# Optimization experiments

Hardware: AMD Instinct MI355X
Metric: run time of the kernel (lower is better)

## Reference

```python
import jax, jax.numpy as jnp
import numpy as np

B, S, E = 2, 2048, 1024
N_HEADS = 16
HEAD_DIM = E // N_HEADS  # 64
ATTN_SCALE = 1.0 / np.sqrt(E)  # NOTE: original scales by 1/sqrt(hidden_dim_phi), not head_dim
ROPE_BASE = 10000.0


def _rope(t):
    # t: (B, H, S, D) with D = HEAD_DIM; interleaved-pair RoPE (torchtune-style)
    d = t.shape[-1]
    s = t.shape[-2]
    inv_freq = 1.0 / (ROPE_BASE ** (jnp.arange(0, d, 2, dtype=jnp.float32) / d))  # (D/2,)
    ang = jnp.arange(s, dtype=jnp.float32)[:, None] * inv_freq[None, :]  # (S, D/2)
    cos, sin = jnp.cos(ang), jnp.sin(ang)  # (S, D/2)
    tp = t.reshape(t.shape[:-1] + (d // 2, 2))
    te, to = tp[..., 0], tp[..., 1]  # (B,H,S,D/2)
    oe = te * cos - to * sin
    oo = te * sin + to * cos
    return jnp.stack([oe, oo], axis=-1).reshape(t.shape)


def setup_inputs() -> dict:
    key = jax.random.key(0)
    ks = jax.random.split(key, 5)
    std = 0.02
    return {
        "x": jax.random.normal(ks[0], (B, S, E), dtype=jnp.float32),
        "W_q": jax.random.normal(ks[1], (E, E), dtype=jnp.float32) * std,
        "W_k": jax.random.normal(ks[2], (E, E), dtype=jnp.float32) * std,
        "W_v": jax.random.normal(ks[3], (E, E), dtype=jnp.float32) * std,
        "W_o": jax.random.normal(ks[4], (E, E), dtype=jnp.float32) * std,
    }


def reference(x, W_q, W_k, W_v, W_o):
    b, s, e = x.shape
    hd = e // N_HEADS
    # projections -> (B, H, S, D)
    def proj(w):
        return (x @ w).reshape(b, s, N_HEADS, hd).transpose(0, 2, 1, 3)
    q = _rope(proj(W_q))
    k = _rope(proj(W_k))
    v = proj(W_v)
    scores = jnp.einsum('bhsd,bhtd->bhst', q, k) * ATTN_SCALE  # (B,H,S,S)
    causal = jnp.triu(jnp.ones((s, s), dtype=bool), k=1)
    scores = jnp.where(causal, -jnp.inf, scores)
    probs = jax.nn.softmax(scores, axis=-1)  # dropout is identity in eval mode
    out = jnp.einsum('bhst,bhtd->bhsd', probs, v)
    out = out.transpose(0, 2, 1, 3).reshape(b, s, e)
    return out @ W_o
```

## Files before the change

kernel.cpp:

```cpp
#include <hip/hip_runtime.h>
#include <hip/hip_bf16.h>

#define S_LEN 2048
#define E_DIM 1024
#define NH 16
#define HD 64
#define ATTN_SCALE 0.03125f
#define QSCALE_L2E 0.045084312f

typedef __attribute__((ext_vector_type(8))) short short8;
typedef __attribute__((ext_vector_type(8))) unsigned short ushort8;
typedef __attribute__((ext_vector_type(4))) unsigned short ushort4_t;
typedef __attribute__((ext_vector_type(4))) float f32x4;
typedef __attribute__((ext_vector_type(16))) float f32x16;
typedef __attribute__((ext_vector_type(4))) float f4;
typedef __attribute__((ext_vector_type(4))) unsigned int uint4v;

__device__ __forceinline__ float bf2f(unsigned short u) {
    unsigned int x = ((unsigned int)u) << 16;
    return __builtin_bit_cast(float, x);
}
__device__ __forceinline__ unsigned short f2bf(float f) {
    unsigned int x = __builtin_bit_cast(unsigned int, f);
    x += 0x7FFFu + ((x >> 16) & 1u);
    return (unsigned short)(x >> 16);
}
__device__ __forceinline__ float exp2_fast(float x) {
    float r;
    asm("v_exp_f32 %0, %1" : "=v"(r) : "v"(x));
    return r;
}
__device__ __forceinline__ void gload16(const unsigned short* g, unsigned short* l) {
    __builtin_amdgcn_global_load_lds(
        (__attribute__((address_space(1))) void*)g,
        (__attribute__((address_space(3))) void*)l, 16, 0, 0);
}

__global__ __launch_bounds__(256) void k_convert(const float* __restrict__ x,
                                                 unsigned short* __restrict__ xb) {
    size_t i = ((size_t)blockIdx.x * 256 + threadIdx.x) * 8;
    f4 a = *(const f4*)(x + i);
    f4 b = *(const f4*)(x + i + 4);
    ushort8 o;
    o[0] = f2bf(a[0]); o[1] = f2bf(a[1]); o[2] = f2bf(a[2]); o[3] = f2bf(a[3]);
    o[4] = f2bf(b[0]); o[5] = f2bf(b[1]); o[6] = f2bf(b[2]); o[7] = f2bf(b[3]);
    *(ushort8*)(xb + i) = o;
}

__global__ __launch_bounds__(256) void k_transw(const float* W0, const float* W1,
                                                const float* W2, const float* W3,
                                                unsigned short* T0, unsigned short* T1,
                                                unsigned short* T2, unsigned short* T3) {
    const float* W; unsigned short* T;
    switch (blockIdx.z) {
        case 0: W = W0; T = T0; break;
        case 1: W = W1; T = T1; break;
        case 2: W = W2; T = T2; break;
        default: W = W3; T = T3; break;
    }
    __shared__ float tile[32][33];
    int tx = threadIdx.x, ty = threadIdx.y;
    int bx = blockIdx.x * 32, by = blockIdx.y * 32;
#pragma unroll
    for (int i = 0; i < 4; i++)
        tile[ty + i * 8][tx] = W[(size_t)(by + ty + i * 8) * E_DIM + bx + tx];
    __syncthreads();
#pragma unroll
    for (int i = 0; i < 4; i++)
        T[(size_t)(bx + ty + i * 8) * E_DIM + by + tx] = f2bf(tile[tx][ty + i * 8]);
}

__global__ __launch_bounds__(256) void k_rope_table(float* __restrict__ cosT,
                                                    float* __restrict__ sinT) {
    int idx = blockIdx.x * 256 + threadIdx.x;
    int s = idx >> 5, j = idx & 31;
    float inv = expf(-(float)j * (9.210340371976184f / 32.f));
    float ang = (float)s * inv;
    cosT[idx] = cosf(ang);
    sinT[idx] = sinf(ang);
}

template <int BM, int BN, int NBN, bool QKV3>
__global__ __launch_bounds__(256, 3)
void k_gemmN(const unsigned short* __restrict__ A,
             const unsigned short* __restrict__ B,
             unsigned short* __restrict__ Qo,
             unsigned short* __restrict__ Ko,
             unsigned short* __restrict__ Vto,
             float* __restrict__ Fo,
             const float* __restrict__ cosT,
             const float* __restrict__ sinT) {
    constexpr int THREADS = 256;
    constexpr int WM = BM / 2, WN = BN / 2;
    constexpr int FM = WM / 16, FN = WN / 16;
    constexpr int NT = E_DIM / 64;
    constexpr int AR = BM * 8 / THREADS;
    constexpr int BR = BN * 8 / THREADS;
    constexpr int STG = AR + BR;
    constexpr int NWG = (4096 / BM) * NBN;
    __shared__ unsigned short Al[2][BM * 64];
    __shared__ unsigned short Bl[2][BN * 64];
    int tid = threadIdx.x, lane = tid & 63, wid = tid >> 6;
    int l15 = lane & 15, lg = lane >> 4;
    int wr = wid >> 1, wc = wid & 1;
    int orig = blockIdx.y * NBN + blockIdx.x;
    int wg = (orig & 7) * (NWG / 8) + (orig >> 3);
    int bm = wg / NBN, bn = wg % NBN;

    auto stage = [&](int buf, int k0) {
#pragma unroll
        for (int i = 0; i < AR; i++) {
            int r = i * (THREADS / 8) + wid * 8 + (lane >> 3);
            int cs = (lane & 7) ^ (r & 7);
            gload16(A + (size_t)(bm * BM + r) * E_DIM + k0 + cs * 8,
                    &Al[buf][i * (THREADS * 8) + wid * 512]);
        }
#pragma unroll
        for (int i = 0; i < BR; i++) {
            int r = i * (THREADS / 8) + wid * 8 + (lane >> 3);
            int cs = (lane & 7) ^ (r & 7);
            gload16(B + (size_t)(bn * BN + r) * E_DIM + k0 + cs * 8,
                    &Bl[buf][i * (THREADS * 8) + wid * 512]);
        }
    };

    f32x4 acc[FM][FN] = {};
    stage(0, 0);
    for (int t = 0; t < NT; t++) {
        int cur = t & 1;
        if (t + 1 < NT) {
            stage(cur ^ 1, (t + 1) * 64);
            asm volatile("s_waitcnt vmcnt(%0)" :: "n"(STG) : "memory");
        } else {
            asm volatile("s_waitcnt vmcnt(0)" ::: "memory");
        }
        __builtin_amdgcn_s_barrier();
        __builtin_amdgcn_sched_barrier(0);
#pragma unroll
        for (int ks = 0; ks < 2; ks++) {
            short8 af[FM], bfv[FN];
#pragma unroll
            for (int m = 0; m < FM; m++) {
                int r = wr * WM + m * 16 + l15;
                int gc = ks * 4 + lg;
                af[m] = *(const short8*)&Al[cur][r * 64 + ((gc ^ (r & 7)) << 3)];
            }
#pragma unroll
            for (int n = 0; n < FN; n++) {
                int r = wc * WN + n * 16 + l15;
                int gc = ks * 4 + lg;
                bfv[n] = *(const short8*)&Bl[cur][r * 64 + ((gc ^ (r & 7)) << 3)];
            }
            __builtin_amdgcn_s_setprio(1);
#pragma unroll
            for (int m = 0; m < FM; m++)
#pragma unroll
                for (int n = 0; n < FN; n++)
                    acc[m][n] = __builtin_amdgcn_mfma_f32_16x16x32_bf16(
                        af[m], bfv[n], acc[m][n], 0, 0, 0);
            __builtin_amdgcn_s_setprio(0);
        }
        __builtin_amdgcn_s_barrier();
    }
#pragma unroll
    for (int m = 0; m < FM; m++) {
        int r0 = bm * BM + wr * WM + m * 16 + lg * 4;
#pragma unroll
        for (int n = 0; n < FN; n++) {
            int colg = bn * BN + wc * WN + n * 16 + l15;
            if (QKV3) {
                int z = colg >> 10, c1 = colg & 1023;
                if (z == 2) {
                    int h = c1 >> 6, d = c1 & 63;
                    int bb = r0 >> 11, s = r0 & 2047;
                    ushort4_t p;
#pragma unroll
                    for (int r = 0; r < 4; r++) p[r] = f2bf(acc[m][n][r]);
                    *(ushort4_t*)(Vto + (((size_t)((bb * 16 + h) * 64 + d)) << 11) + s) = p;
                } else {
                    unsigned short* T = z ? Ko : Qo;
                    int dl = c1 & 63, j = dl >> 1;
                    float sgn = (dl & 1) ? 1.f : -1.f;
                    float scq = z ? 1.f : QSCALE_L2E;
#pragma unroll
                    for (int r = 0; r < 4; r++) {
                        int row = r0 + r, s = row & 2047;
                        float c = cosT[s * 32 + j], sn = sinT[s * 32 + j];
                        float v = acc[m][n][r];
                        float p = __shfl_xor(v, 1);
                        T[(size_t)row * E_DIM + c1] = f2bf((v * c + sgn * p * sn) * scq);
                    }
                }
            } else {
#pragma unroll
                for (int r = 0; r < 4; r++)
                    Fo[(size_t)(r0 + r) * E_DIM + colg] = acc[m][n][r];
            }
        }
    }
}

__global__ __launch_bounds__(128, 2)
void k_attn32(const unsigned short* __restrict__ Q,
              const unsigned short* __restrict__ K,
              const unsigned short* __restrict__ Vt,
              unsigned short* __restrict__ O) {
    __shared__ unsigned short K_lds[2][4096];
    __shared__ unsigned short V_lds[2][4096];
    int tid = threadIdx.x, lane = tid & 63, wid = tid >> 6;
    int l31 = lane & 31, hi = lane >> 5;
    int orig = blockIdx.y * 32 + blockIdx.x;
    int xcd = orig & 7, idx = orig >> 3;
    int u = idx & 31, v = idx >> 5;
    int bh = xcd * 4 + v;
    int p = (v & 1) ? (31 - u) : u;
    int b = bh >> 4, h = bh & 15;
    const size_t base_qk = (size_t)b * S_LEN * E_DIM + (size_t)h * HD;
    const unsigned short* Vbh = Vt + ((size_t)(bh * 64) << 11);

    auto stageK = [&](int buf, int kt) {
#pragma unroll
        for (int i = 0; i < 4; i++) {
            int r = i * 16 + (tid >> 3);
            int cs = (tid & 7) ^ (r & 7);
            gload16(K + base_qk + (size_t)(kt * 64 + r) * E_DIM + cs * 8,
                    &K_lds[buf][i * 1024 + tid * 8]);
        }
    };
    auto stageV = [&](int buf, int kt) {
#pragma unroll
        for (int i = 0; i < 4; i++) {
            int r = i * 16 + (tid >> 3);
            int cs = (tid & 7) ^ (r & 7);
            gload16(Vbh + (size_t)r * 2048 + kt * 64 + cs * 8,
                    &V_lds[buf][i * 1024 + tid * 8]);
        }
    };

    int q_glob = p * 64 + wid * 32 + l31;
    const unsigned short* Qb = Q + base_qk + (size_t)q_glob * E_DIM;
    short8 qf[4];
#pragma unroll
    for (int s = 0; s < 4; s++)
        qf[s] = *(const short8*)(Qb + s * 16 + hi * 8);

    f32x16 ot0 = {}, ot1 = {};
    float m_i = -1e30f, l_i = 0.f;
    int nkt = p + 1;
    int swz = l31 & 7;
    stageK(0, 0);
    stageV(0, 0);
    asm volatile("s_waitcnt vmcnt(0)" ::: "memory");
    __builtin_amdgcn_s_barrier();
    __builtin_amdgcn_sched_barrier(0);
    int cur = 0;
    for (int kt = 0; kt < nkt; ++kt) {
        if (kt + 1 < nkt) {
            stageK(cur ^ 1, kt + 1);
            stageV(cur ^ 1, kt + 1);
        }
        f32x16 st0 = {}, st1 = {};
        __builtin_amdgcn_s_setprio(1);
#pragma unroll
        for (int s = 0; s < 4; s++) {
            int c = ((s * 2 + hi) ^ swz) << 3;
            short8 ka0 = *(const short8*)&K_lds[cur][l31 * 64 + c];
            short8 ka1 = *(const short8*)&K_lds[cur][(32 + l31) * 64 + c];
            st0 = __builtin_amdgcn_mfma_f32_32x32x16_bf16(ka0, qf[s], st0, 0, 0, 0);
            st1 = __builtin_amdgcn_mfma_f32_32x32x16_bf16(ka1, qf[s], st1, 0, 0, 0);
        }
        __builtin_amdgcn_s_setprio(0);
        float p0[16], p1[16];
        float vmax = -1e30f;
        if (kt == nkt - 1) {
#pragma unroll
            for (int r = 0; r < 16; r++) {
                int kg = kt * 64 + (r & 3) + 8 * (r >> 2) + 4 * hi;
                float v0 = (kg > q_glob) ? -1e30f : st0[r];
                float v1 = (kg + 32 > q_glob) ? -1e30f : st1[r];
                p0[r] = v0; p1[r] = v1;
                vmax = fmaxf(vmax, fmaxf(v0, v1));
            }
        } else {
#pragma unroll
            for (int r = 0; r < 16; r++) {
                p0[r] = st0[r]; p1[r] = st1[r];
                vmax = fmaxf(vmax, fmaxf(st0[r], st1[r]));
            }
        }
        vmax = fmaxf(vmax, __shfl_xor(vmax, 32));
        float m_new = fmaxf(m_i, vmax);
        float corr = exp2_fast(m_i - m_new);
        float rs = 0.f;
#pragma unroll
        for (int r = 0; r < 16; r++) {
            p0[r] = exp2_fast(p0[r] - m_new);
            p1[r] = exp2_fast(p1[r] - m_new);
            rs += p0[r] + p1[r];
        }
        rs += __shfl_xor(rs, 32);
        l_i = l_i * corr + rs;
        m_i = m_new;
#pragma unroll
        for (int r = 0; r < 16; r++) { ot0[r] *= corr; ot1[r] *= corr; }
        unsigned int pk0[8], pk1[8];
#pragma unroll
        for (int i = 0; i < 8; i++) {
            asm("v_cvt_pk_bf16_f32 %0, %1, %2"
                : "=v"(pk0[i]) : "v"(p0[2 * i]), "v"(p0[2 * i + 1]));
            asm("v_cvt_pk_bf16_f32 %0, %1, %2"
                : "=v"(pk1[i]) : "v"(p1[2 * i]), "v"(p1[2 * i + 1]));
        }
        bool ishi = hi != 0;
        __builtin_amdgcn_s_setprio(1);
#pragma unroll
        for (int kk = 0; kk < 4; kk++) {
            const unsigned int* pkt = (kk & 2) ? pk1 : pk0;
            int off = (kk & 1) * 4;
            unsigned int a  = pkt[off + 0], b2 = pkt[off + 1];
            unsigned int c2 = pkt[off + 2], d2 = pkt[off + 3];
            unsigned int sa = __shfl_xor(a, 32),  sb = __shfl_xor(b2, 32);
            unsigned int sc = __shfl_xor(c2, 32), sd = __shfl_xor(d2, 32);
            uint4v w;
            w[0] = ishi ? sc : a;  w[1] = ishi ? sd : b2;
            w[2] = ishi ? c2 : sa; w[3] = ishi ? d2 : sb;
            short8 pf = __builtin_bit_cast(short8, w);
            int cv = ((kk * 2 + hi) ^ swz) << 3;
            short8 va0 = *(const short8*)&V_lds[cur][l31 * 64 + cv];
            short8 va1 = *(const short8*)&V_lds[cur][(32 + l31) * 64 + cv];
            ot0 = __builtin_amdgcn_mfma_f32_32x32x16_bf16(va0, pf, ot0, 0, 0, 0);
            ot1 = __builtin_amdgcn_mfma_f32_32x32x16_bf16(va1, pf, ot1, 0, 0, 0);
        }
        __builtin_amdgcn_s_setprio(0);
        asm volatile("s_waitcnt vmcnt(0)" ::: "memory");
        __builtin_amdgcn_s_barrier();
        __builtin_amdgcn_sched_barrier(0);
        cur ^= 1;
    }
    __builtin_amdgcn_s_barrier();
    float linv = 1.f / l_i;
    unsigned short* scb = &K_lds[0][0] + wid * 2304;
#pragma unroll
    for (int i = 0; i < 8; i++) {
        int d = 2 * (i & 1) + 8 * (i >> 1) + 4 * hi;
        unsigned int w0, w1;
        float a0 = ot0[2 * i] * linv, a1 = ot0[2 * i + 1] * linv;
        float b0 = ot1[2 * i] * linv, b1 = ot1[2 * i + 1] * linv;
        asm("v_cvt_pk_bf16_f32 %0, %1, %2" : "=v"(w0) : "v"(a0), "v"(a1));
        asm("v_cvt_pk_bf16_f32 %0, %1, %2" : "=v"(w1) : "v"(b0), "v"(b1));
        *(unsigned int*)&scb[l31 * 72 + d] = w0;
        *(unsigned int*)&scb[l31 * 72 + 32 + d] = w1;
    }
    asm volatile("s_waitcnt lgkmcnt(0)" ::: "memory");
    __builtin_amdgcn_sched_barrier(0);
    int qr = lane >> 1, half = (lane & 1) * 32;
    unsigned short* Ob = O + base_qk + (size_t)(p * 64 + wid * 32 + qr) * E_DIM;
#pragma unroll
    for (int j = 0; j < 4; j++) {
        short8 vv = *(const short8*)&scb[qr * 72 + half + j * 8];
        *(short8*)(Ob + half + j * 8) = vv;
    }
}

extern "C" void kernel_launch(void* const* d_in, const int* in_sizes, int n_in,
                              void* d_out, int out_size, void* d_ws, size_t ws_size,
                              hipStream_t stream) {
    (void)in_sizes; (void)n_in; (void)out_size; (void)ws_size;
    const float* x  = (const float*)d_in[0];
    const float* Wq = (const float*)d_in[1];
    const float* Wk = (const float*)d_in[2];
    const float* Wv = (const float*)d_in[3];
    const float* Wo = (const float*)d_in[4];

    unsigned short* us = (unsigned short*)d_ws;
    unsigned short* xb    = us;
    unsigned short* WqkvT = us + 4194304;
    unsigned short* WoT   = us + 7340032;
    unsigned short* Qb    = us + 8388608;
    unsigned short* Kb    = us + 12582912;
    unsigned short* Vt    = us + 16777216;
    unsigned short* AO    = us + 20971520;
    float* cosT = (float*)((char*)d_ws + 50331648);
    float* sinT = cosT + 65536;

    k_convert<<<2048, 256, 0, stream>>>(x, xb);
    k_transw<<<dim3(32, 32, 4), dim3(32, 8), 0, stream>>>(
        Wq, Wk, Wv, Wo, WqkvT, WqkvT + 1048576, WqkvT + 2097152, WoT);
    k_rope_table<<<256, 256, 0, stream>>>(cosT, sinT);
    k_gemmN<128, 64, 48, true><<<dim3(48, 32), 256, 0, stream>>>(
        xb, WqkvT, Qb, Kb, Vt, nullptr, cosT, sinT);
    k_attn32<<<dim3(32, 32), 128, 0, stream>>>(Qb, Kb, Vt, AO);
    k_gemmN<128, 64, 16, false><<<dim3(16, 32), 256, 0, stream>>>(
        AO, WoT, nullptr, nullptr, nullptr, (float*)d_out, cosT, sinT);
}
```

Measured before the change: 117.7 us.

## Merge prep kernels, retile QKV GEMM, and restructure attention to 128-query blocks

Folds the x conversion, weight transpose and RoPE table kernels into a single prep launch to cut launch overhead. Replaces the double-buffered 128x64 QKV GEMM with a simpler single-buffered 128x128 tile using K-steps of 32 and barriers each step. Rewrites attention so each 4-wave block handles 128 queries sharing one K/V stage, with single-buffered K and V split-staged across phases. Waves whose rows are fully masked skip work. This trades double-buffer prefetch for more K/V reuse per block and fewer blocks, and risks exposed load latency and more barriers.

```diff
diff --git a/kernel.cpp b/kernel.cpp
--- a/kernel.cpp
+++ b/kernel.cpp
@@ -36,60 +36,142 @@
         (__attribute__((address_space(3))) void*)l, 16, 0, 0);
 }
 
-__global__ __launch_bounds__(256) void k_convert(const float* __restrict__ x,
-                                                 unsigned short* __restrict__ xb) {
-    size_t i = ((size_t)blockIdx.x * 256 + threadIdx.x) * 8;
-    f4 a = *(const f4*)(x + i);
-    f4 b = *(const f4*)(x + i + 4);
-    ushort8 o;
-    o[0] = f2bf(a[0]); o[1] = f2bf(a[1]); o[2] = f2bf(a[2]); o[3] = f2bf(a[3]);
-    o[4] = f2bf(b[0]); o[5] = f2bf(b[1]); o[6] = f2bf(b[2]); o[7] = f2bf(b[3]);
-    *(ushort8*)(xb + i) = o;
-}
-
-__global__ __launch_bounds__(256) void k_transw(const float* W0, const float* W1,
-                                                const float* W2, const float* W3,
-                                                unsigned short* T0, unsigned short* T1,
-                                                unsigned short* T2, unsigned short* T3) {
-    const float* W; unsigned short* T;
-    switch (blockIdx.z) {
-        case 0: W = W0; T = T0; break;
-        case 1: W = W1; T = T1; break;
-        case 2: W = W2; T = T2; break;
-        default: W = W3; T = T3; break;
-    }
-    __shared__ float tile[32][33];
-    int tx = threadIdx.x, ty = threadIdx.y;
-    int bx = blockIdx.x * 32, by = blockIdx.y * 32;
-#pragma unroll
-    for (int i = 0; i < 4; i++)
-        tile[ty + i * 8][tx] = W[(size_t)(by + ty + i * 8) * E_DIM + bx + tx];
-    __syncthreads();
-#pragma unroll
-    for (int i = 0; i < 4; i++)
-        T[(size_t)(bx + ty + i * 8) * E_DIM + by + tx] = f2bf(tile[tx][ty + i * 8]);
-}
-
-__global__ __launch_bounds__(256) void k_rope_table(float* __restrict__ cosT,
-                                                    float* __restrict__ sinT) {
-    int idx = blockIdx.x * 256 + threadIdx.x;
-    int s = idx >> 5, j = idx & 31;
-    float inv = expf(-(float)j * (9.210340371976184f / 32.f));
-    float ang = (float)s * inv;
-    cosT[idx] = cosf(ang);
-    sinT[idx] = sinf(ang);
-}
-
-template <int BM, int BN, int NBN, bool QKV3>
+__global__ __launch_bounds__(256) void k_prep(const float* __restrict__ x,
+                                              unsigned short* __restrict__ xb,
+                                              const float* W0, const float* W1,
+                                              const float* W2, const float* W3,
+                                              unsigned short* Tqkv,
+                                              unsigned short* Twout,
+                                              float* __restrict__ cosT,
+                                              float* __restrict__ sinT) {
+    int bid = blockIdx.x;
+    int tid = threadIdx.x;
+    if (bid < 2048) {
+        size_t i = ((size_t)bid * 256 + tid) * 8;
+        f4 a = *(const f4*)(x + i);
+        f4 b = *(const f4*)(x + i + 4);
+        ushort8 o;
+        o[0] = f2bf(a[0]); o[1] = f2bf(a[1]); o[2] = f2bf(a[2]); o[3] = f2bf(a[3]);
+        o[4] = f2bf(b[0]); o[5] = f2bf(b[1]); o[6] = f2bf(b[2]); o[7] = f2bf(b[3]);
+        *(ushort8*)(xb + i) = o;
+    } else if (bid < 2304) {
+        int idx = (bid - 2048) * 256 + tid;
+        int s = idx >> 5, j = idx & 31;
+        float inv = expf(-(float)j * (9.210340371976184f / 32.f));
+        float ang = (float)s * inv;
+        cosT[idx] = cosf(ang);
+        sinT[idx] = sinf(ang);
+    } else {
+        int t = bid - 2304;
+        int bx = (t & 31) * 32, by = ((t >> 5) & 31) * 32, z = t >> 10;
+        const float* W; unsigned short* T;
+        switch (z) {
+            case 0: W = W0; T = Tqkv; break;
+            case 1: W = W1; T = Tqkv + 1048576; break;
+            case 2: W = W2; T = Tqkv + 2097152; break;
+            default: W = W3; T = Twout; break;
+        }
+        __shared__ float tile[32][33];
+        int tx = tid & 31, ty = tid >> 5;
+#pragma unroll
+        for (int i = 0; i < 4; i++)
+            tile[ty + i * 8][tx] = W[(size_t)(by + ty + i * 8) * E_DIM + bx + tx];
+        __syncthreads();
+#pragma unroll
+        for (int i = 0; i < 4; i++)
+            T[(size_t)(bx + ty + i * 8) * E_DIM + by + tx] = f2bf(tile[tx][ty + i * 8]);
+    }
+}
+
 __global__ __launch_bounds__(256, 3)
-void k_gemmN(const unsigned short* __restrict__ A,
+void k_gemm97(const unsigned short* __restrict__ A,
+              const unsigned short* __restrict__ B,
+              unsigned short* __restrict__ Qo,
+              unsigned short* __restrict__ Ko,
+              unsigned short* __restrict__ Vto,
+              const float* __restrict__ cosT,
+              const float* __restrict__ sinT) {
+    constexpr int NBN = 24;
+    constexpr int NWG = 32 * NBN;
+    __shared__ unsigned short Alds[4096];
+    __shared__ unsigned short Blds[4096];
+    int tid = threadIdx.x, lane = tid & 63, wid = tid >> 6;
+    int l15 = lane & 15, lg = lane >> 4;
+    int wr = wid >> 1, wc = wid & 1;
+    int orig = blockIdx.y * NBN + blockIdx.x;
+    int wg = (orig & 7) * (NWG / 8) + (orig >> 3);
+    int bm = wg / NBN, bn = wg % NBN;
+    int c0 = wid * 2, c1c = wid * 2 + 1;
+    int srow0 = c0 * 16 + (lane >> 2);
+    int srow1 = c1c * 16 + (lane >> 2);
+    int scol = (lane & 3) * 8;
+    const unsigned short* As0 = A + (size_t)(bm * 128 + srow0) * E_DIM + scol;
+    const unsigned short* As1 = A + (size_t)(bm * 128 + srow1) * E_DIM + scol;
+    const unsigned short* Bs0 = B + (size_t)(bn * 128 + srow0) * E_DIM + scol;
+    const unsigned short* Bs1 = B + (size_t)(bn * 128 + srow1) * E_DIM + scol;
+    unsigned short* Ad0 = Alds + c0 * 512;
+    unsigned short* Ad1 = Alds + c1c * 512;
+    unsigned short* Bd0 = Blds + c0 * 512;
+    unsigned short* Bd1 = Blds + c1c * 512;
+    f32x4 acc[4][4] = {};
+    for (int k0 = 0; k0 < E_DIM; k0 += 32) {
+        gload16(As0 + k0, Ad0);
+        gload16(As1 + k0, Ad1);
+        gload16(Bs0 + k0, Bd0);
+        gload16(Bs1 + k0, Bd1);
+        __syncthreads();
+        short8 af[4], bfr[4];
+#pragma unroll
+        for (int mf = 0; mf < 4; mf++)
+            af[mf] = *(const short8*)(Alds + (wr * 64 + mf * 16 + l15) * 32 + lg * 8);
+#pragma unroll
+        for (int nf = 0; nf < 4; nf++)
+            bfr[nf] = *(const short8*)(Blds + (wc * 64 + nf * 16 + l15) * 32 + lg * 8);
+#pragma unroll
+        for (int mf = 0; mf < 4; mf++)
+#pragma unroll
+            for (int nf = 0; nf < 4; nf++)
+                acc[mf][nf] = __builtin_amdgcn_mfma_f32_16x16x32_bf16(
+                    af[mf], bfr[nf], acc[mf][nf], 0, 0, 0);
+        __syncthreads();
+    }
+#pragma unroll
+    for (int mf = 0; mf < 4; mf++) {
+        int r0 = bm * 128 + wr * 64 + mf * 16 + lg * 4;
+#pragma unroll
+        for (int nf = 0; nf < 4; nf++) {
+            int colg = bn * 128 + wc * 64 + nf * 16 + l15;
+            int z = colg >> 10, c1 = colg & 1023;
+            if (z == 2) {
+                int h = c1 >> 6, d = c1 & 63;
+                int bb = r0 >> 11, s = r0 & 2047;
+                ushort4_t p;
+#pragma unroll
+                for (int r = 0; r < 4; r++) p[r] = f2bf(acc[mf][nf][r]);
+                *(ushort4_t*)(Vto + (((size_t)((bb * 16 + h) * 64 + d)) << 11) + s) = p;
+            } else {
+                unsigned short* T = z ? Ko : Qo;
+                int dl = c1 & 63, j = dl >> 1;
+                float sgn = (dl & 1) ? 1.f : -1.f;
+                float scq = z ? 1.f : QSCALE_L2E;
+#pragma unroll
+                for (int r = 0; r < 4; r++) {
+                    int row = r0 + r, s = row & 2047;
+                    float c = cosT[s * 32 + j], sn = sinT[s * 32 + j];
+                    float v = acc[mf][nf][r];
+                    float p = __shfl_xor(v, 1);
+                    T[(size_t)row * E_DIM + c1] = f2bf((v * c + sgn * p * sn) * scq);
+                }
+            }
+        }
+    }
+}
+
+template <int BM, int BN, int NBN>
+__global__ __launch_bounds__(256, 3)
+void k_gemmo(const unsigned short* __restrict__ A,
              const unsigned short* __restrict__ B,
-             unsigned short* __restrict__ Qo,
-             unsigned short* __restrict__ Ko,
-             unsigned short* __restrict__ Vto,
-             float* __restrict__ Fo,
-             const float* __restrict__ cosT,
-             const float* __restrict__ sinT) {
+             float* __restrict__ Fo) {
     constexpr int THREADS = 256;
     constexpr int WM = BM / 2, WN = BN / 2;
     constexpr int FM = WM / 16, FN = WN / 16;
@@ -168,178 +250,171 @@
 #pragma unroll
         for (int n = 0; n < FN; n++) {
             int colg = bn * BN + wc * WN + n * 16 + l15;
-            if (QKV3) {
-                int z = colg >> 10, c1 = colg & 1023;
-                if (z == 2) {
-                    int h = c1 >> 6, d = c1 & 63;
-                    int bb = r0 >> 11, s = r0 & 2047;
-                    ushort4_t p;
-#pragma unroll
-                    for (int r = 0; r < 4; r++) p[r] = f2bf(acc[m][n][r]);
-                    *(ushort4_t*)(Vto + (((size_t)((bb * 16 + h) * 64 + d)) << 11) + s) = p;
-                } else {
-                    unsigned short* T = z ? Ko : Qo;
-                    int dl = c1 & 63, j = dl >> 1;
-                    float sgn = (dl & 1) ? 1.f : -1.f;
-                    float scq = z ? 1.f : QSCALE_L2E;
-#pragma unroll
-                    for (int r = 0; r < 4; r++) {
-                        int row = r0 + r, s = row & 2047;
-                        float c = cosT[s * 32 + j], sn = sinT[s * 32 + j];
-                        float v = acc[m][n][r];
-                        float p = __shfl_xor(v, 1);
-                        T[(size_t)row * E_DIM + c1] = f2bf((v * c + sgn * p * sn) * scq);
-                    }
-                }
-            } else {
-#pragma unroll
-                for (int r = 0; r < 4; r++)
-                    Fo[(size_t)(r0 + r) * E_DIM + colg] = acc[m][n][r];
-            }
-        }
-    }
-}
-
-__global__ __launch_bounds__(128, 2)
-void k_attn32(const unsigned short* __restrict__ Q,
-              const unsigned short* __restrict__ K,
-              const unsigned short* __restrict__ Vt,
-              unsigned short* __restrict__ O) {
-    __shared__ unsigned short K_lds[2][4096];
-    __shared__ unsigned short V_lds[2][4096];
+#pragma unroll
+            for (int r = 0; r < 4; r++)
+                Fo[(size_t)(r0 + r) * E_DIM + colg] = acc[m][n][r];
+        }
+    }
+}
+
+__global__ __launch_bounds__(256, 3)
+void k_attn9(const unsigned short* __restrict__ Q,
+             const unsigned short* __restrict__ K,
+             const unsigned short* __restrict__ Vt,
+             unsigned short* __restrict__ O) {
+    __shared__ unsigned short lds[9216];
+    unsigned short* Klds = lds;
+    unsigned short* Vlds = lds + 4096;
     int tid = threadIdx.x, lane = tid & 63, wid = tid >> 6;
     int l31 = lane & 31, hi = lane >> 5;
-    int orig = blockIdx.y * 32 + blockIdx.x;
+    int orig = blockIdx.y * 16 + blockIdx.x;
     int xcd = orig & 7, idx = orig >> 3;
-    int u = idx & 31, v = idx >> 5;
-    int bh = xcd * 4 + v;
-    int p = (v & 1) ? (31 - u) : u;
+    int bh = xcd * 4 + (idx & 3);
+    int j = idx >> 2;
+    int pt = (j < 8) ? (15 - j) : (j - 8);
     int b = bh >> 4, h = bh & 15;
     const size_t base_qk = (size_t)b * S_LEN * E_DIM + (size_t)h * HD;
     const unsigned short* Vbh = Vt + ((size_t)(bh * 64) << 11);
 
-    auto stageK = [&](int buf, int kt) {
-#pragma unroll
-        for (int i = 0; i < 4; i++) {
-            int r = i * 16 + (tid >> 3);
+    int qbase = pt * 128 + wid * 32;
+    int q_glob = qbase + l31;
+    int nkt = 2 * pt + 2;
+
+    const unsigned short* Qb = Q + base_qk + (size_t)q_glob * E_DIM;
+    short8 qf[4];
+#pragma unroll
+    for (int s = 0; s < 4; s++)
+        qf[s] = *(const short8*)(Qb + s * 16 + hi * 8);
+
+    auto stageK = [&](int kt) {
+        const unsigned short* Kb = K + base_qk + (size_t)(kt * 64) * E_DIM;
+#pragma unroll
+        for (int i = 0; i < 2; i++) {
+            int r = i * 32 + (tid >> 3);
             int cs = (tid & 7) ^ (r & 7);
-            gload16(K + base_qk + (size_t)(kt * 64 + r) * E_DIM + cs * 8,
-                    &K_lds[buf][i * 1024 + tid * 8]);
+            gload16(Kb + (size_t)r * E_DIM + cs * 8, Klds + i * 2048 + tid * 8);
         }
     };
-    auto stageV = [&](int buf, int kt) {
-#pragma unroll
-        for (int i = 0; i < 4; i++) {
-            int r = i * 16 + (tid >> 3);
+    auto stageV = [&](int kt) {
+#pragma unroll
+        for (int i = 0; i < 2; i++) {
+            int r = i * 32 + (tid >> 3);
             int cs = (tid & 7) ^ (r & 7);
             gload16(Vbh + (size_t)r * 2048 + kt * 64 + cs * 8,
-                    &V_lds[buf][i * 1024 + tid * 8]);
+                    Vlds + i * 2048 + tid * 8);
         }
     };
-
-    int q_glob = p * 64 + wid * 32 + l31;
-    const unsigned short* Qb = Q + base_qk + (size_t)q_glob * E_DIM;
-    short8 qf[4];
-#pragma unroll
-    for (int s = 0; s < 4; s++)
-        qf[s] = *(const short8*)(Qb + s * 16 + hi * 8);
 
     f32x16 ot0 = {}, ot1 = {};
     float m_i = -1e30f, l_i = 0.f;
-    int nkt = p + 1;
     int swz = l31 & 7;
-    stageK(0, 0);
-    stageV(0, 0);
-    asm volatile("s_waitcnt vmcnt(0)" ::: "memory");
+
+    stageK(0);
+    stageV(0);
+    asm volatile("s_waitcnt vmcnt(2)" ::: "memory");
     __builtin_amdgcn_s_barrier();
     __builtin_amdgcn_sched_barrier(0);
-    int cur = 0;
     for (int kt = 0; kt < nkt; ++kt) {
+        bool active = (kt * 64) <= (qbase + 31);
+        f32x16 st0 = {}, st1 = {};
+        if (active) {
+            __builtin_amdgcn_s_setprio(1);
+#pragma unroll
+            for (int s = 0; s < 4; s++) {
+                int c = ((s * 2 + hi) ^ swz) << 3;
+                short8 ka0 = *(const short8*)&Klds[l31 * 64 + c];
+                short8 ka1 = *(const short8*)&Klds[(32 + l31) * 64 + c];
+                st0 = __builtin_amdgcn_mfma_f32_32x32x16_bf16(ka0, qf[s], st0, 0, 0, 0);
+                st1 = __builtin_amdgcn_mfma_f32_32x32x16_bf16(ka1, qf[s], st1, 0, 0, 0);
+            }
+            __builtin_amdgcn_s_setprio(0);
+        }
+        __builtin_amdgcn_s_barrier();
+        if (kt + 1 < nkt) stageK(kt + 1);
+        unsigned int pk0[8], pk1[8];
+        if (active) {
+            float p0[16], p1[16];
+            float vmax = -1e30f;
+            bool domask = (kt * 64 + 63) > qbase;
+            if (domask) {
+#pragma unroll
+                for (int r = 0; r < 16; r++) {
+                    int kg = kt * 64 + (r & 3) + 8 * (r >> 2) + 4 * hi;
+                    float v0 = (kg > q_glob) ? -1e30f : st0[r];
+                    float v1 = (kg + 32 > q_glob) ? -1e30f : st1[r];
+                    p0[r] = v0; p1[r] = v1;
+                    vmax = fmaxf(vmax, fmaxf(v0, v1));
+                }
+            } else {
+#pragma unroll
+                for (int r = 0; r < 16; r++) {
+                    p0[r] = st0[r]; p1[r] = st1[r];
+                    vmax = fmaxf(vmax, fmaxf(st0[r], st1[r]));
+                }
+            }
+            vmax = fmaxf(vmax, __shfl_xor(vmax, 32));
+            float m_new = fmaxf(m_i, vmax);
+            float corr = exp2_fast(m_i - m_new);
+            float rs = 0.f;
+#pragma unroll
+            for (int r = 0; r < 16; r++) {
+                p0[r] = exp2_fast(p0[r] - m_new);
+                p1[r] = exp2_fast(p1[r] - m_new);
+                rs += p0[r] + p1[r];
+            }
+            rs += __shfl_xor(rs, 32);
+            l_i = l_i * corr + rs;
+            m_i = m_new;
+#pragma unroll
+            for (int r = 0; r < 16; r++) { ot0[r] *= corr; ot1[r] *= corr; }
+#pragma unroll
+            for (int i = 0; i < 8; i++) {
+                asm("v_cvt_pk_bf16_f32 %0, %1, %2"
+                    : "=v"(pk0[i]) : "v"(p0[2 * i]), "v"(p0[2 * i + 1]));
+                asm("v_cvt_pk_bf16_f32 %0, %1, %2"
+                    : "=v"(pk1[i]) : "v"(p1[2 * i]), "v"(p1[2 * i + 1]));
+            }
+        }
+        if (kt + 1 < nkt)
+            asm volatile("s_waitcnt vmcnt(2)" ::: "memory");
+        else
+            asm volatile("s_waitcnt vmcnt(0)" ::: "memory");
+        __builtin_amdgcn_s_barrier();
+        __builtin_amdgcn_sched_barrier(0);
+        if (active) {
+            bool ishi = hi != 0;
+            __builtin_amdgcn_s_setprio(1);
+#pragma unroll
+            for (int kk = 0; kk < 4; kk++) {
+                const unsigned int* pkt = (kk & 2) ? pk1 : pk0;
+                int off = (kk & 1) * 4;
+                unsigned int a  = pkt[off + 0], b2 = pkt[off + 1];
+                unsigned int c2 = pkt[off + 2], d2 = pkt[off + 3];
+                unsigned int sa = __shfl_xor(a, 32),  sb = __shfl_xor(b2, 32);
+                unsigned int sc = __shfl_xor(c2, 32), sd = __shfl_xor(d2, 32);
+                uint4v w;
+                w[0] = ishi ? sc : a;  w[1] = ishi ? sd : b2;
+                w[2] = ishi ? c2 : sa; w[3] = ishi ? d2 : sb;
+                short8 pf = __builtin_bit_cast(short8, w);
+                int cv = ((kk * 2 + hi) ^ swz) << 3;
+                short8 va0 = *(const short8*)&Vlds[l31 * 64 + cv];
+                short8 va1 = *(const short8*)&Vlds[(32 + l31) * 64 + cv];
+                ot0 = __builtin_amdgcn_mfma_f32_32x32x16_bf16(va0, pf, ot0, 0, 0, 0);
+                ot1 = __builtin_amdgcn_mfma_f32_32x32x16_bf16(va1, pf, ot1, 0, 0, 0);
+            }
+            __builtin_amdgcn_s_setprio(0);
+        }
+        __builtin_amdgcn_s_barrier();
         if (kt + 1 < nkt) {
-            stageK(cur ^ 1, kt + 1);
-            stageV(cur ^ 1, kt + 1);
-        }
-        f32x16 st0 = {}, st1 = {};
-        __builtin_amdgcn_s_setprio(1);
-#pragma unroll
-        for (int s = 0; s < 4; s++) {
-            int c = ((s * 2 + hi) ^ swz) << 3;
-            short8 ka0 = *(const short8*)&K_lds[cur][l31 * 64 + c];
-            short8 ka1 = *(const short8*)&K_lds[cur][(32 + l31) * 64 + c];
-            st0 = __builtin_amdgcn_mfma_f32_32x32x16_bf16(ka0, qf[s], st0, 0, 0, 0);
-            st1 = __builtin_amdgcn_mfma_f32_32x32x16_bf16(ka1, qf[s], st1, 0, 0, 0);
-        }
-        __builtin_amdgcn_s_setprio(0);
-        float p0[16], p1[16];
-        float vmax = -1e30f;
-        if (kt == nkt - 1) {
-#pragma unroll
-            for (int r = 0; r < 16; r++) {
-                int kg = kt * 64 + (r & 3) + 8 * (r >> 2) + 4 * hi;
-                float v0 = (kg > q_glob) ? -1e30f : st0[r];
-                float v1 = (kg + 32 > q_glob) ? -1e30f : st1[r];
-                p0[r] = v0; p1[r] = v1;
-                vmax = fmaxf(vmax, fmaxf(v0, v1));
-            }
-        } else {
-#pragma unroll
-            for (int r = 0; r < 16; r++) {
-                p0[r] = st0[r]; p1[r] = st1[r];
-                vmax = fmaxf(vmax, fmaxf(st0[r], st1[r]));
-            }
-        }
-        vmax = fmaxf(vmax, __shfl_xor(vmax, 32));
-        float m_new = fmaxf(m_i, vmax);
-        float corr = exp2_fast(m_i - m_new);
-        float rs = 0.f;
-#pragma unroll
-        for (int r = 0; r < 16; r++) {
-            p0[r] = exp2_fast(p0[r] - m_new);
-            p1[r] = exp2_fast(p1[r] - m_new);
-            rs += p0[r] + p1[r];
-        }
-        rs += __shfl_xor(rs, 32);
-        l_i = l_i * corr + rs;
-        m_i = m_new;
-#pragma unroll
-        for (int r = 0; r < 16; r++) { ot0[r] *= corr; ot1[r] *= corr; }
-        unsigned int pk0[8], pk1[8];
-#pragma unroll
-        for (int i = 0; i < 8; i++) {
-            asm("v_cvt_pk_bf16_f32 %0, %1, %2"
-                : "=v"(pk0[i]) : "v"(p0[2 * i]), "v"(p0[2 * i + 1]));
-            asm("v_cvt_pk_bf16_f32 %0, %1, %2"
-                : "=v"(pk1[i]) : "v"(p1[2 * i]), "v"(p1[2 * i + 1]));
-        }
-        bool ishi = hi != 0;
-        __builtin_amdgcn_s_setprio(1);
-#pragma unroll
-        for (int kk = 0; kk < 4; kk++) {
-            const unsigned int* pkt = (kk & 2) ? pk1 : pk0;
-            int off = (kk & 1) * 4;
-            unsigned int a  = pkt[off + 0], b2 = pkt[off + 1];
-            unsigned int c2 = pkt[off + 2], d2 = pkt[off + 3];
-            unsigned int sa = __shfl_xor(a, 32),  sb = __shfl_xor(b2, 32);
-            unsigned int sc = __shfl_xor(c2, 32), sd = __shfl_xor(d2, 32);
-            uint4v w;
-            w[0] = ishi ? sc : a;  w[1] = ishi ? sd : b2;
-            w[2] = ishi ? c2 : sa; w[3] = ishi ? d2 : sb;
-            short8 pf = __builtin_bit_cast(short8, w);
-            int cv = ((kk * 2 + hi) ^ swz) << 3;
-            short8 va0 = *(const short8*)&V_lds[cur][l31 * 64 + cv];
-            short8 va1 = *(const short8*)&V_lds[cur][(32 + l31) * 64 + cv];
-            ot0 = __builtin_amdgcn_mfma_f32_32x32x16_bf16(va0, pf, ot0, 0, 0, 0);
-            ot1 = __builtin_amdgcn_mfma_f32_32x32x16_bf16(va1, pf, ot1, 0, 0, 0);
-        }
-        __builtin_amdgcn_s_setprio(0);
-        asm volatile("s_waitcnt vmcnt(0)" ::: "memory");
+            stageV(kt + 1);
+            asm volatile("s_waitcnt vmcnt(2)" ::: "memory");
+        }
         __builtin_amdgcn_s_barrier();
         __builtin_amdgcn_sched_barrier(0);
-        cur ^= 1;
     }
     __builtin_amdgcn_s_barrier();
     float linv = 1.f / l_i;
-    unsigned short* scb = &K_lds[0][0] + wid * 2304;
+    unsigned short* scb = lds + wid * 2304;
 #pragma unroll
     for (int i = 0; i < 8; i++) {
         int d = 2 * (i & 1) + 8 * (i >> 1) + 4 * hi;
@@ -354,11 +429,11 @@
     asm volatile("s_waitcnt lgkmcnt(0)" ::: "memory");
     __builtin_amdgcn_sched_barrier(0);
     int qr = lane >> 1, half = (lane & 1) * 32;
-    unsigned short* Ob = O + base_qk + (size_t)(p * 64 + wid * 32 + qr) * E_DIM;
-#pragma unroll
-    for (int j = 0; j < 4; j++) {
-        short8 vv = *(const short8*)&scb[qr * 72 + half + j * 8];
-        *(short8*)(Ob + half + j * 8) = vv;
+    unsigned short* Ob = O + base_qk + (size_t)(qbase + qr) * E_DIM;
+#pragma unroll
+    for (int jj = 0; jj < 4; jj++) {
+        short8 vv = *(const short8*)&scb[qr * 72 + half + jj * 8];
+        *(short8*)(Ob + half + jj * 8) = vv;
     }
 }
 
@@ -383,13 +458,8 @@
     float* cosT = (float*)((char*)d_ws + 50331648);
     float* sinT = cosT + 65536;
 
-    k_convert<<<2048, 256, 0, stream>>>(x, xb);
-    k_transw<<<dim3(32, 32, 4), dim3(32, 8), 0, stream>>>(
-        Wq, Wk, Wv, Wo, WqkvT, WqkvT + 1048576, WqkvT + 2097152, WoT);
-    k_rope_table<<<256, 256, 0, stream>>>(cosT, sinT);
-    k_gemmN<128, 64, 48, true><<<dim3(48, 32), 256, 0, stream>>>(
-        xb, WqkvT, Qb, Kb, Vt, nullptr, cosT, sinT);
-    k_attn32<<<dim3(32, 32), 128, 0, stream>>>(Qb, Kb, Vt, AO);
-    k_gemmN<128, 64, 16, false><<<dim3(16, 32), 256, 0, stream>>>(
-        AO, WoT, nullptr, nullptr, nullptr, (float*)d_out, cosT, sinT);
-}
+    k_prep<<<6400, 256, 0, stream>>>(x, xb, Wq, Wk, Wv, Wo, WqkvT, WoT, cosT, sinT);
+    k_gemm97<<<dim3(24, 32), 256, 0, stream>>>(xb, WqkvT, Qb, Kb, Vt, cosT, sinT);
+    k_attn9<<<dim3(16, 32), 256, 0, stream>>>(Qb, Kb, Vt, AO);
+    k_gemmo<128, 64, 16><<<dim3(16, 32), 256, 0, stream>>>(AO, WoT, (float*)d_out);
+}
```

Measured after the change: 114.5 us. -2.7%, faster.
